# Kernel tuning notes

Measured on AMD Instinct MI355X. Metric: run time of the kernel, lower is better.

## Reference

```python
import jax, jax.numpy as jnp
import numpy as np

B, I, T = 8192, 128, 21
H1, H2, H3 = 256, 256, 128


def _init(key, shape, fan_in):
    # torch-style uniform(-1/sqrt(fan_in), 1/sqrt(fan_in))
    bound = 1.0 / np.sqrt(fan_in)
    return jax.random.uniform(key, shape, jnp.float32, -bound, bound)


def setup_inputs() -> dict:
    key = jax.random.key(0)
    ks = jax.random.split(key, 16)
    x = jax.random.normal(ks[0], (B, I, T), jnp.float32)
    d = {"x": x}
    # stacked LSTM weights (PyTorch layout: W_ih (4H, in), gate order i,f,g,o)
    d["W1_ih"] = _init(ks[1], (4 * H1, I), H1)
    d["b1_ih"] = _init(ks[2], (4 * H1,), H1)
    d["b1_hh"] = _init(ks[3], (4 * H1,), H1)
    d["W2_ih"] = _init(ks[4], (4 * H2, H1), H2)
    d["b2_ih"] = _init(ks[5], (4 * H2,), H2)
    d["b2_hh"] = _init(ks[6], (4 * H2,), H2)
    d["W3_ih"] = _init(ks[7], (4 * H3, H2), H3)
    d["b3_ih"] = _init(ks[8], (4 * H3,), H3)
    d["b3_hh"] = _init(ks[9], (4 * H3,), H3)
    d["fc1_w"] = _init(ks[10], (1, H3), H3)
    d["fc1_b"] = _init(ks[11], (1,), H3)
    d["fc2_w"] = _init(ks[12], (T, T), T)
    d["fc2_b"] = _init(ks[13], (T,), T)
    return d


def _lstm_cell_step(xt, W_ih, b_ih, b_hh):
    # single timestep with h0 = c0 = 0, so the W_hh @ h0 term vanishes
    gates = xt @ W_ih.T + (b_ih + b_hh)          # (B, 21, 4H)
    i, f, g, o = jnp.split(gates, 4, axis=-1)    # torch gate order i,f,g,o
    c = jax.nn.sigmoid(i) * jnp.tanh(g)          # f * c0 = 0
    return jax.nn.sigmoid(o) * jnp.tanh(c)


def reference(x, W1_ih, b1_ih, b1_hh, W2_ih, b2_ih, b2_hh,
              W3_ih, b3_ih, b3_hh, fc1_w, fc1_b, fc2_w, fc2_b):
    # fold the 21 independent single-step columns into the batch dim
    xt = jnp.transpose(x, (0, 2, 1))             # (B, 21, I)
    h1 = _lstm_cell_step(xt, W1_ih, b1_ih, b1_hh)   # (B, 21, H1)
    h2 = _lstm_cell_step(h1, W2_ih, b2_ih, b2_hh)   # (B, 21, H2)
    h3 = _lstm_cell_step(h2, W3_ih, b3_ih, b3_hh)   # (B, 21, H3)
    y = h3 @ fc1_w.T + fc1_b                     # (B, 21, 1)
    y = y[..., 0][:, None, :]                    # (B, 1, 21)  == x_torch
    out = y @ fc2_w.T + fc2_b                    # (B, 1, 21)
    return out
```

## Files before the change

### kernel.cpp

```cpp
#include <hip/hip_runtime.h>
#include <hip/hip_bf16.h>
#include <stdint.h>


typedef __attribute__((ext_vector_type(8))) short bf16x8;
typedef __attribute__((ext_vector_type(4))) float f32x4;

#define M_ROWS 172032
#define BATCH  8192

__device__ __forceinline__ float bf2f(unsigned short u) {
    union { unsigned int i; float f; } v; v.i = ((unsigned int)u) << 16; return v.f;
}
__device__ __forceinline__ unsigned short f2bf(float f) {
    union { float f; unsigned int i; } v; v.f = f;
    unsigned int r = v.i + 0x7fffu + ((v.i >> 16) & 1u);
    return (unsigned short)(r >> 16);
}

#define LOG2E  1.44269504f
#define LOG2E2 2.88539008f

__device__ __forceinline__ float lstm_h(float gi, float gg, float go) {
    gg = fminf(fmaxf(gg, -15.0f), 15.0f);
    float Eg = __builtin_amdgcn_exp2f(gg * LOG2E2);
    float Ei = __builtin_amdgcn_exp2f(-gi * LOG2E);
    float c  = (Eg - 1.0f) * __builtin_amdgcn_rcpf((Eg + 1.0f) * (1.0f + Ei));
    float Eo = __builtin_amdgcn_exp2f(-go * LOG2E);
    float c2 = c * c;
    float num = c * fmaf(c2, c2 + 105.0f, 945.0f);
    float den = fmaf(c2, fmaf(15.0f, c2, 420.0f), 945.0f);
    return num * __builtin_amdgcn_rcpf(den * (1.0f + Eo));
}

__device__ __forceinline__ void gload_lds16(const unsigned short* g, unsigned short* l) {
    __builtin_amdgcn_global_load_lds(
        (const __attribute__((address_space(1))) unsigned int*)g,
        (__attribute__((address_space(3))) unsigned int*)l,
        16, 0, 0);
}

__global__ __launch_bounds__(256) void k_convert(
    const float* __restrict__ src, unsigned short* __restrict__ dst, int n4)
{
    int i = blockIdx.x * 256 + threadIdx.x;
    if (i < n4) {
        float4 v = ((const float4*)src)[i];
        ushort4 o;
        o.x = f2bf(v.x); o.y = f2bf(v.y); o.z = f2bf(v.z); o.w = f2bf(v.w);
        ((ushort4*)dst)[i] = o;
    }
}

__global__ __launch_bounds__(256) void k_transpose(
    const float* __restrict__ x, unsigned short* __restrict__ xt)
{
    __shared__ unsigned short tile[128 * 22];
    const int b = blockIdx.x, tid = threadIdx.x;
    const float* xb = x + (size_t)b * 2688;
    for (int idx = tid; idx < 2688; idx += 256) {
        int i = idx / 21, t = idx - i * 21;
        tile[i * 22 + t] = f2bf(xb[idx]);
    }
    __syncthreads();
    unsigned short* xtb = xt + (size_t)b * 2688;
    for (int idx = tid; idx < 2688; idx += 256) {
        int t = idx >> 7, i = idx & 127;
        xtb[t * 128 + i] = tile[i * 22 + t];
    }
}

template<int K, int HG>
__global__ __launch_bounds__(256, 2) void k_gemm_act(
    const unsigned short* __restrict__ A,
    const unsigned short* __restrict__ W,
    const float* __restrict__ bih,
    const float* __restrict__ bhh,
    unsigned short* __restrict__ Hout)
{
    __shared__ __align__(16) unsigned short As[128 * 64];
    __shared__ __align__(16) unsigned short Ws[192 * 64];

    const int tid  = threadIdx.x;
    const int wave = tid >> 6;
    const int lane = tid & 63;
    const int wm = wave >> 1;
    const int wn = wave & 1;
    const int r0 = blockIdx.x * 128;
    const int c0 = blockIdx.y * 64;
    const int csel = lane & 15;

    const unsigned short* aptr[4];
#pragma unroll
    for (int i = 0; i < 4; ++i) {
        int q16 = (wave * 4 + i) * 64 + lane;
        int row = q16 >> 3, pslot = q16 & 7;
        int lslot = pslot ^ (row & 7);
        aptr[i] = A + (size_t)(r0 + row) * K + lslot * 8;
    }
    const unsigned short* wptr[6];
#pragma unroll
    for (int i = 0; i < 6; ++i) {
        int q16 = (wave * 6 + i) * 64 + lane;
        int lrow = q16 >> 3, pslot = q16 & 7;
        int lslot = pslot ^ (lrow & 7);
        int gate = lrow >> 6, n = lrow & 63;
        int gbase = (gate == 0) ? 0 : (gate + 1) * HG;
        wptr[i] = W + (size_t)(gbase + c0 + n) * K + lslot * 8;
    }

    float bias[3][2];
#pragma unroll
    for (int n = 0; n < 2; ++n) {
        int cloc = c0 + wn * 32 + n * 16 + csel;
        bias[0][n] = bih[cloc] + bhh[cloc];
        bias[1][n] = bih[2 * HG + cloc] + bhh[2 * HG + cloc];
        bias[2][n] = bih[3 * HG + cloc] + bhh[3 * HG + cloc];
    }

    f32x4 acc[3][4][2];
#pragma unroll
    for (int g = 0; g < 3; ++g)
#pragma unroll
        for (int m = 0; m < 4; ++m)
#pragma unroll
            for (int n = 0; n < 2; ++n)
                acc[g][m][n] = (f32x4){0.f, 0.f, 0.f, 0.f};

#pragma unroll
    for (int kk = 0; kk < K; kk += 64) {
        if (kk) __syncthreads();
#pragma unroll
        for (int i = 0; i < 4; ++i)
            gload_lds16(aptr[i] + kk, &As[(wave * 4 + i) * 512]);
#pragma unroll
        for (int i = 0; i < 6; ++i)
            gload_lds16(wptr[i] + kk, &Ws[(wave * 6 + i) * 512]);
        __syncthreads();

#pragma unroll
        for (int ks = 0; ks < 64; ks += 32) {
            bf16x8 af[4];
            bf16x8 bfr[3][2];
            const int rsel = lane & 15;
            const int slot = (ks >> 3) | (lane >> 4);
            const int soff = (slot ^ (rsel & 7)) * 8;
#pragma unroll
            for (int m = 0; m < 4; ++m)
                af[m] = *(const bf16x8*)&As[(wm * 64 + m * 16 + rsel) * 64 + soff];
#pragma unroll
            for (int g = 0; g < 3; ++g)
#pragma unroll
                for (int n = 0; n < 2; ++n)
                    bfr[g][n] = *(const bf16x8*)&Ws[(g * 64 + wn * 32 + n * 16 + rsel) * 64 + soff];
#pragma unroll
            for (int g = 0; g < 3; ++g)
#pragma unroll
                for (int m = 0; m < 4; ++m)
#pragma unroll
                    for (int n = 0; n < 2; ++n)
                        acc[g][m][n] = __builtin_amdgcn_mfma_f32_16x16x32_bf16(
                            af[m], bfr[g][n], acc[g][m][n], 0, 0, 0);
        }
    }

    const int quad = lane >> 4;
#pragma unroll
    for (int m = 0; m < 4; ++m) {
#pragma unroll
        for (int n = 0; n < 2; ++n) {
            int cloc = wn * 32 + n * 16 + csel;
            f32x4 vi = acc[0][m][n], vg = acc[1][m][n], vo = acc[2][m][n];
#pragma unroll
            for (int r = 0; r < 4; ++r) {
                int row = r0 + wm * 64 + m * 16 + quad * 4 + r;
                float h = lstm_h(vi[r] + bias[0][n], vg[r] + bias[1][n],
                                 vo[r] + bias[2][n]);
                Hout[(size_t)row * HG + c0 + cloc] = f2bf(h);
            }
        }
    }
}

#define FSTR 169
__global__ __launch_bounds__(256) void k_final(
    const unsigned short* __restrict__ h3,
    const float* __restrict__ fc1w,
    const float* __restrict__ fc1b,
    const float* __restrict__ fc2w,
    const float* __restrict__ fc2b,
    float* __restrict__ out)
{
    __shared__ unsigned short ht[128 * FSTR];
    __shared__ float fwl[128];
    __shared__ float yl[168];
    __shared__ float f2l[441];
    __shared__ float f2bl[21];

    const int tid = threadIdx.x;
    const int b0 = blockIdx.x * 8;

    if (tid < 128) fwl[tid] = fc1w[tid];
    for (int i = tid; i < 441; i += 256) f2l[i] = fc2w[i];
    if (tid < 21) f2bl[tid] = fc2b[tid];

    const unsigned int* hsrc = (const unsigned int*)(h3 + (size_t)b0 * 2688);
    for (int gi = tid; gi < 10752; gi += 256) {
        unsigned int v = hsrc[gi];
        int e = gi * 2;
        int task = e >> 7;
        int c = e & 127;
        ht[c * FSTR + task] = (unsigned short)(v & 0xffffu);
        ht[(c + 1) * FSTR + task] = (unsigned short)(v >> 16);
    }
    __syncthreads();

    const float f1b = fc1b[0];
    if (tid < 168) {
        float s = f1b;
#pragma unroll 8
        for (int c = 0; c < 128; ++c)
            s += fwl[c] * bf2f(ht[c * FSTR + tid]);
        yl[tid] = s;
    }
    __syncthreads();
    if (tid < 168) {
        int bloc = tid / 21;
        int tp = tid - bloc * 21;
        float s = f2bl[tp];
#pragma unroll
        for (int t = 0; t < 21; ++t)
            s += yl[bloc * 21 + t] * f2l[tp * 21 + t];
        out[(size_t)(b0 + bloc) * 21 + tp] = s;
    }
}

extern "C" void kernel_launch(void* const* d_in, const int* in_sizes, int n_in,
                              void* d_out, int out_size, void* d_ws, size_t ws_size,
                              hipStream_t stream)
{
    const float* x    = (const float*)d_in[0];
    const float* W1   = (const float*)d_in[1];
    const float* b1i  = (const float*)d_in[2];
    const float* b1h  = (const float*)d_in[3];
    const float* W2   = (const float*)d_in[4];
    const float* b2i  = (const float*)d_in[5];
    const float* b2h  = (const float*)d_in[6];
    const float* W3   = (const float*)d_in[7];
    const float* b3i  = (const float*)d_in[8];
    const float* b3h  = (const float*)d_in[9];
    const float* fc1w = (const float*)d_in[10];
    const float* fc1b = (const float*)d_in[11];
    const float* fc2w = (const float*)d_in[12];
    const float* fc2b = (const float*)d_in[13];
    float* out = (float*)d_out;

    unsigned short* Wc1 = (unsigned short*)d_ws;
    unsigned short* Wc2 = Wc1 + 131072;
    unsigned short* Wc3 = Wc2 + 262144;
    unsigned short* buf = Wc3 + 131072;

    int C = 1;
    while (C < 64 && 1048576 + (size_t)(M_ROWS / C) * 1536 > ws_size) C <<= 1;
    const int R  = M_ROWS / C;
    const int Bc = BATCH / C;

    unsigned short* xt = buf;
    unsigned short* h1 = xt + (size_t)R * 128;
    unsigned short* h2 = h1 + (size_t)R * 256;
    unsigned short* h3 = h2 + (size_t)R * 256;

    k_convert<<<128, 256, 0, stream>>>(W1, Wc1, 32768);
    k_convert<<<256, 256, 0, stream>>>(W2, Wc2, 65536);
    k_convert<<<128, 256, 0, stream>>>(W3, Wc3, 32768);

    for (int c = 0; c < C; ++c) {
        const float* xc = x + (size_t)c * Bc * 2688;
        k_transpose<<<Bc, 256, 0, stream>>>(xc, xt);
        k_gemm_act<128, 256><<<dim3(R / 128, 4), 256, 0, stream>>>(xt, Wc1, b1i, b1h, h1);
        k_gemm_act<256, 256><<<dim3(R / 128, 4), 256, 0, stream>>>(h1, Wc2, b2i, b2h, h2);
        k_gemm_act<256, 128><<<dim3(R / 128, 2), 256, 0, stream>>>(h2, Wc3, b3i, b3h, h3);
        k_final<<<Bc / 8, 256, 0, stream>>>(h3, fc1w, fc1b, fc2w, fc2b,
                                            out + (size_t)c * Bc * 21);
    }
}
```

Before: 406.2 us.

## Fuse weight conversions, vectorize transpose I/O, and remap GEMM block order

Merges the three weight-conversion launches into one kernel, cutting launch overhead. The transpose kernel now reads with float4 loads and writes packed pairs of bf16 values, so it issues fewer, wider memory operations. The GEMM kernels remap block indices so that all column blocks of a 336-row-block segment are scheduled together, which is meant to improve L2 reuse of the A tiles. The transpose adds divisions and branches per element, and the remap only applies when gridDim.x is a multiple of 336.

```diff
diff --git a/kernel.cpp b/kernel.cpp
--- a/kernel.cpp
+++ b/kernel.cpp
@@ -40,16 +40,21 @@
         16, 0, 0);
 }
 
-__global__ __launch_bounds__(256) void k_convert(
-    const float* __restrict__ src, unsigned short* __restrict__ dst, int n4)
+__global__ __launch_bounds__(256) void k_convert3(
+    const float* __restrict__ W1, const float* __restrict__ W2,
+    const float* __restrict__ W3,
+    unsigned short* __restrict__ d1, unsigned short* __restrict__ d2,
+    unsigned short* __restrict__ d3)
 {
     int i = blockIdx.x * 256 + threadIdx.x;
-    if (i < n4) {
-        float4 v = ((const float4*)src)[i];
-        ushort4 o;
-        o.x = f2bf(v.x); o.y = f2bf(v.y); o.z = f2bf(v.z); o.w = f2bf(v.w);
-        ((ushort4*)dst)[i] = o;
-    }
+    const float* src; unsigned short* dst; int off;
+    if (i < 32768)      { src = W1; dst = d1; off = i; }
+    else if (i < 98304) { src = W2; dst = d2; off = i - 32768; }
+    else                { src = W3; dst = d3; off = i - 98304; }
+    float4 v = ((const float4*)src)[off];
+    ushort4 o;
+    o.x = f2bf(v.x); o.y = f2bf(v.y); o.z = f2bf(v.z); o.w = f2bf(v.w);
+    ((ushort4*)dst)[off] = o;
 }
 
 __global__ __launch_bounds__(256) void k_transpose(
@@ -57,16 +62,25 @@
 {
     __shared__ unsigned short tile[128 * 22];
     const int b = blockIdx.x, tid = threadIdx.x;
-    const float* xb = x + (size_t)b * 2688;
-    for (int idx = tid; idx < 2688; idx += 256) {
-        int i = idx / 21, t = idx - i * 21;
-        tile[i * 22 + t] = f2bf(xb[idx]);
+    const float4* xb4 = (const float4*)(x + (size_t)b * 2688);
+    for (int j = tid; j < 672; j += 256) {
+        float4 v = xb4[j];
+        int e = j * 4;
+        int ii = e / 21, tt = e - ii * 21;
+        float vv[4] = {v.x, v.y, v.z, v.w};
+#pragma unroll
+        for (int k = 0; k < 4; ++k) {
+            tile[ii * 22 + tt] = f2bf(vv[k]);
+            if (++tt == 21) { tt = 0; ++ii; }
+        }
     }
     __syncthreads();
-    unsigned short* xtb = xt + (size_t)b * 2688;
-    for (int idx = tid; idx < 2688; idx += 256) {
-        int t = idx >> 7, i = idx & 127;
-        xtb[t * 128 + i] = tile[i * 22 + t];
+    unsigned int* xtb = (unsigned int*)(xt + (size_t)b * 2688);
+    for (int idx = tid; idx < 1344; idx += 256) {
+        int t = idx >> 6, i2 = (idx & 63) * 2;
+        unsigned int lo = tile[i2 * 22 + t];
+        unsigned int hi = tile[(i2 + 1) * 22 + t];
+        xtb[t * 64 + (idx & 63)] = lo | (hi << 16);
     }
 }
 
@@ -86,9 +100,20 @@
     const int lane = tid & 63;
     const int wm = wave >> 1;
     const int wn = wave & 1;
-    const int r0 = blockIdx.x * 128;
-    const int c0 = blockIdx.y * 64;
     const int csel = lane & 15;
+
+    int bx = blockIdx.x, by = blockIdx.y;
+    if ((gridDim.x % 336) == 0) {
+        int ny = gridDim.y;
+        int lin = by * gridDim.x + bx;
+        int segblocks = 336 * ny;
+        int seg = lin / segblocks;
+        int rem = lin - seg * segblocks;
+        by = rem / 336;
+        bx = seg * 336 + (rem - by * 336);
+    }
+    const int r0 = bx * 128;
+    const int c0 = by * 64;
 
     const unsigned short* aptr[4];
 #pragma unroll
@@ -270,9 +295,7 @@
     unsigned short* h2 = h1 + (size_t)R * 256;
     unsigned short* h3 = h2 + (size_t)R * 256;
 
-    k_convert<<<128, 256, 0, stream>>>(W1, Wc1, 32768);
-    k_convert<<<256, 256, 0, stream>>>(W2, Wc2, 65536);
-    k_convert<<<128, 256, 0, stream>>>(W3, Wc3, 32768);
+    k_convert3<<<512, 256, 0, stream>>>(W1, W2, W3, Wc1, Wc2, Wc3);
 
     for (int c = 0; c < C; ++c) {
         const float* xc = x + (size_t)c * Bc * 2688;
```

Result: no change. 404.0 us (-0.6%).
